# Kernel optimization log

Measured on AMD Instinct MI355X. Metric: run time of the kernel, lower is better.

Reference implementation:

```python
import jax, jax.numpy as jnp
import numpy as np

CUTOFFS = [16000, 28000, 36000]
HID = 1024
PROJ = [256, 64]  # hidden/4**1, hidden/4**2 per compute_proj_dims
CLUSTERS = 2


def setup_inputs() -> dict:
    key = jax.random.key(0)
    ks = jax.random.split(key, 12)
    B, S = 4, 1024
    scale = 0.02
    d = {
        "inp": jax.random.normal(ks[0], (B, S, HID), jnp.float32),
        "labels": jax.random.randint(ks[1], (B, S), 0, CUTOFFS[-1]),
        "head_W": jax.random.normal(ks[2], (HID, CUTOFFS[0] + CLUSTERS), jnp.float32) * scale,
        "head_b": jnp.zeros((CUTOFFS[0] + CLUSTERS,), jnp.float32),
    }
    for i in range(CLUSTERS):
        tdim = CUTOFFS[i + 1] - CUTOFFS[i]
        d[f"t{i}_pW"] = jax.random.normal(ks[3 + 4 * i], (HID, PROJ[i]), jnp.float32) * scale
        d[f"t{i}_pb"] = jnp.zeros((PROJ[i],), jnp.float32)
        d[f"t{i}_W"] = jax.random.normal(ks[4 + 4 * i], (PROJ[i], CUTOFFS[i + 1] - CUTOFFS[i]), jnp.float32) * scale
        d[f"t{i}_b"] = jnp.zeros((CUTOFFS[i + 1] - CUTOFFS[i],), jnp.float32)
    return d


def _sparse_ce(logits, labels):
    # stable sparse softmax cross entropy, single log_softmax pass
    logp = jax.nn.log_softmax(logits, axis=-1)
    return -jnp.take_along_axis(logp, labels[..., None], axis=-1)[..., 0]


def reference(inp, labels, head_W, head_b, t0_pW, t0_pb, t0_W, t0_b, t1_pW, t1_pb, t1_W, t1_b):
    tails = [(t0_pW, t0_pb, t0_W, t0_b), (t1_pW, t1_pb, t1_W, t1_b)]
    head_labels = labels
    loss = jnp.zeros(labels.shape, inp.dtype)
    for i, (pW, pb, W, b) in enumerate(tails):
        lo, hi = CUTOFFS[i], CUTOFFS[i + 1]
        mask = (labels >= lo) & (labels < hi)
        # tokens in cluster i are relabeled to cluster id in the head
        head_labels = jnp.where(mask, CUTOFFS[0] + i, head_labels)
        # two-layer tail projection: [B,S,H] -> [B,S,proj] -> [B,S,tail_dim]
        tail_logits = (inp @ pW + pb) @ W + b
        tail_labels = jnp.clip(labels - lo, 0, hi - lo - 1)
        loss = loss + jnp.where(mask, _sparse_ce(tail_logits, tail_labels), 0.0)
    head_logits = inp @ head_W + head_b  # [B,S,cutoffs[0]+clusters]
    loss = _sparse_ce(head_logits, head_labels) + loss
    loss = loss * (labels != 0).astype(loss.dtype)  # zero out pad positions
    return jnp.mean(loss)
```

## Files before the change

### kernel.cpp

```cpp
#include <hip/hip_runtime.h>
#include <hip/hip_bf16.h>
#include <hip/hip_fp8.h>
#include <cstdint>
#include <cstddef>

#define M_TOK 4096
#define HID   1024
#define NHEAD 16002
#define NHEAD_PAD 16128
#define P0    256
#define N0    12000
#define N0_PAD 12032
#define P1    64
#define N1    8000
#define N1_PAD 8192
#define PFUSE 384
#define PREAL 320

typedef unsigned char u8;
typedef float f32x4 __attribute__((ext_vector_type(4)));
typedef int   i32x4 __attribute__((ext_vector_type(4)));
typedef int   i32x8 __attribute__((ext_vector_type(8)));

__device__ __forceinline__ void load16(const void* g, void* l) {
    __builtin_amdgcn_global_load_lds(
        (__attribute__((address_space(1))) void*)g,
        (__attribute__((address_space(3))) void*)l,
        16, 0, 0);
}

__device__ __forceinline__ u8 to_e4m3(float f) {
    __hip_fp8_e4m3 h(f);
    return (u8)h.__x;
}

template <bool LSEP>
__device__ __forceinline__ void gemm_body(
        const u8* __restrict__ A, int lda, const u8* __restrict__ BT, int ldb,
        const float* __restrict__ bias, int K, int realN,
        const int* __restrict__ tgt, float* __restrict__ sumexp, float* __restrict__ lab,
        u8* __restrict__ out, int ldo, int m0, int n0,
        u8* As, u8* Bs) {
    const int tid  = threadIdx.x;
    const int lane = tid & 63;
    const int wave = tid >> 6;
    const int wm = wave >> 1, wn = wave & 1;
    const int q = lane >> 4, lrow = lane & 15;
    const int sw = lrow & 7;

    int aofs[4], bofs[4];
    #pragma unroll
    for (int p = 0; p < 4; p++) {
        int pg = wave * 256 + p * 64 + lane;
        int row = pg >> 3, gcol = (pg & 7) ^ (row & 7);
        aofs[p] = row * lda + gcol * 16;
        bofs[p] = row * ldb + gcol * 16;
    }

    f32x4 acc[4][4];
    #pragma unroll
    for (int mt = 0; mt < 4; mt++)
        #pragma unroll
        for (int nt = 0; nt < 4; nt++)
            acc[mt][nt] = (f32x4)(0.0f);

    const u8* Ab = A  + (size_t)m0 * lda;
    const u8* Bb = BT + (size_t)n0 * ldb;

    union Frag { struct { i32x4 lo, hi; } half; i32x8 v; };

    const int aLo = ((wm * 64 + lrow) * 8 + ((2 * q)     ^ sw)) * 16;
    const int aHi = ((wm * 64 + lrow) * 8 + ((2 * q + 1) ^ sw)) * 16;
    const int bLo = ((wn * 64 + lrow) * 8 + ((2 * q)     ^ sw)) * 16;
    const int bHi = ((wn * 64 + lrow) * 8 + ((2 * q + 1) ^ sw)) * 16;

    for (int k0 = 0; k0 < K; k0 += 128) {
        #pragma unroll
        for (int p = 0; p < 4; p++) {
            int base = (wave * 256 + p * 64) * 16;
            load16(Ab + k0 + aofs[p], As + base);
            load16(Bb + k0 + bofs[p], Bs + base);
        }
        __syncthreads();

        Frag fb[4];
        #pragma unroll
        for (int t = 0; t < 4; t++) {
            fb[t].half.lo = *reinterpret_cast<const i32x4*>(Bs + bLo + t * 2048);
            fb[t].half.hi = *reinterpret_cast<const i32x4*>(Bs + bHi + t * 2048);
        }
        Frag fA[2];
        fA[0].half.lo = *reinterpret_cast<const i32x4*>(As + aLo);
        fA[0].half.hi = *reinterpret_cast<const i32x4*>(As + aHi);
        #pragma unroll
        for (int mt = 0; mt < 4; mt++) {
            if (mt < 3) {
                fA[(mt + 1) & 1].half.lo = *reinterpret_cast<const i32x4*>(As + aLo + (mt + 1) * 2048);
                fA[(mt + 1) & 1].half.hi = *reinterpret_cast<const i32x4*>(As + aHi + (mt + 1) * 2048);
            }
            #pragma unroll
            for (int nt = 0; nt < 4; nt++)
                acc[mt][nt] = __builtin_amdgcn_mfma_scale_f32_16x16x128_f8f6f4(
                    fA[mt & 1].v, fb[nt].v, acc[mt][nt],
                    0, 0,
                    0, 0x7F7F7F7F,
                    0, 0x7A7A7A7A);
        }
        __syncthreads();
    }

    int colg[4]; float bias_v[4];
    #pragma unroll
    for (int nt = 0; nt < 4; nt++) {
        colg[nt] = n0 + wn * 64 + nt * 16 + lrow;
        bias_v[nt] = (colg[nt] < realN) ? bias[colg[nt]] : 0.0f;
    }

    #pragma unroll
    for (int mt = 0; mt < 4; mt++) {
        int rowb = m0 + wm * 64 + mt * 16 + q * 4;
        #pragma unroll
        for (int r = 0; r < 4; r++) {
            int tok = rowb + r;
            if constexpr (LSEP) {
                int tg = tgt[tok];
                float s = 0.0f;
                #pragma unroll
                for (int nt = 0; nt < 4; nt++) {
                    if (colg[nt] < realN) {
                        float logit = acc[mt][nt][r] + bias_v[nt];
                        s += __expf(logit);
                        if (colg[nt] == tg) atomicAdd(&lab[tok], logit);
                    }
                }
                s += __shfl_xor(s, 1);
                s += __shfl_xor(s, 2);
                s += __shfl_xor(s, 4);
                s += __shfl_xor(s, 8);
                if (lrow == 0) atomicAdd(&sumexp[tok], s);
            } else {
                #pragma unroll
                for (int nt = 0; nt < 4; nt++)
                    out[(size_t)tok * ldo + colg[nt]] = to_e4m3(acc[mt][nt][r] + bias_v[nt]);
            }
        }
    }
}

__launch_bounds__(256, 4)
__global__ void gemm_proj(const u8* __restrict__ A, const u8* __restrict__ BT,
                          const float* __restrict__ bias, u8* __restrict__ out) {
    __shared__ __align__(16) u8 As[16384];
    __shared__ __align__(16) u8 Bs[16384];
    gemm_body<false>(A, HID, BT, HID, bias, HID, PREAL,
                     nullptr, nullptr, nullptr, out, PFUSE,
                     blockIdx.x * 128, blockIdx.y * 128, As, Bs);
}

struct Seg {
    const u8* A; int lda;
    const u8* BT; int ldb;
    const float* bias; int K; int realN;
    const int* tgt; float* sumexp; float* lab;
    int nblk;
};

__launch_bounds__(256, 4)
__global__ void gemm_lse3(Seg s0, Seg s1, Seg s2) {
    __shared__ __align__(16) u8 As[16384];
    __shared__ __align__(16) u8 Bs[16384];
    int b = blockIdx.x;
    Seg s; int rel;
    if (b < s0.nblk)                { s = s0; rel = b; }
    else if (b < s0.nblk + s1.nblk) { s = s1; rel = b - s0.nblk; }
    else                            { s = s2; rel = b - s0.nblk - s1.nblk; }
    int pair = rel >> 6, inner = rel & 63;
    int m0 = (inner >> 1) * 128;
    int n0 = (pair * 2 + (inner & 1)) * 128;
    gemm_body<true>(s.A, s.lda, s.BT, s.ldb, s.bias, s.K, s.realN,
                    s.tgt, s.sumexp, s.lab, nullptr, 0, m0, n0, As, Bs);
}

__device__ __forceinline__ void do_transpose(const float* __restrict__ W, u8* __restrict__ WT,
                                             int K, int N, int Kpad, float scale,
                                             int bx, int by, float (*tile)[65]) {
    int n0 = bx * 64, k0 = by * 64;
    int tx = threadIdx.x & 63, ty = threadIdx.x >> 6;
    #pragma unroll
    for (int i = 0; i < 16; i++) {
        int k = k0 + ty + i * 4, n = n0 + tx;
        tile[ty + i * 4][tx] = (k < K && n < N) ? W[(size_t)k * N + n] * scale : 0.0f;
    }
    __syncthreads();
    int n = threadIdx.x >> 2, kb = (threadIdx.x & 3) * 16;
    union { u8 b[16]; uint4 u; } v;
    #pragma unroll
    for (int j = 0; j < 16; j++) v.b[j] = to_e4m3(tile[kb + j][n]);
    *reinterpret_cast<uint4*>(WT + (size_t)(n0 + n) * Kpad + k0 + kb) = v.u;
}

#define NBT_HEAD 4032
#define NBT_CAST 1024
#define NBT_T0W   752
#define NBT_T1W   256
#define NBT_T0P    64
#define NBT_T1P    32
#define NBT_INIT   16

__global__ void prep_kernel(const float* __restrict__ inp, const int* __restrict__ labels,
                            const float* __restrict__ head_W,
                            const float* __restrict__ t0_pW, const float* __restrict__ t0_pb,
                            const float* __restrict__ t0_W,
                            const float* __restrict__ t1_pW, const float* __restrict__ t1_pb,
                            const float* __restrict__ t1_W,
                            u8* __restrict__ inp_f8, u8* __restrict__ headW8,
                            u8* __restrict__ fpW8, u8* __restrict__ t0W8, u8* __restrict__ t1W8,
                            float* __restrict__ acc6, int* __restrict__ tgts,
                            float* __restrict__ pbias, float* __restrict__ out) {
    __shared__ float tile[64][65];
    int b = blockIdx.x;
    if (b < NBT_HEAD) {
        do_transpose(head_W, headW8, HID, NHEAD, HID, 32.0f, b % 252, b / 252, tile);
    } else if (b < NBT_HEAD + NBT_CAST) {
        int r = b - NBT_HEAD;
        int i = r * 256 + threadIdx.x;
        float4 v = reinterpret_cast<const float4*>(inp)[i];
        uchar4 o8;
        o8.x = to_e4m3(v.x); o8.y = to_e4m3(v.y); o8.z = to_e4m3(v.z); o8.w = to_e4m3(v.w);
        reinterpret_cast<uchar4*>(inp_f8)[i] = o8;
    } else if (b < NBT_HEAD + NBT_CAST + NBT_T0W) {
        int r = b - (NBT_HEAD + NBT_CAST);
        do_transpose(t0_W, t0W8, P0, N0, P0, 32.0f, r % 188, r / 188, tile);
    } else if (b < NBT_HEAD + NBT_CAST + NBT_T0W + NBT_T1W) {
        int r = b - (NBT_HEAD + NBT_CAST + NBT_T0W);
        do_transpose(t1_W, t1W8, P1, N1, 128, 32.0f, r % 128, r / 128, tile);
    } else if (b < NBT_HEAD + NBT_CAST + NBT_T0W + NBT_T1W + NBT_T0P) {
        int r = b - (NBT_HEAD + NBT_CAST + NBT_T0W + NBT_T1W);
        do_transpose(t0_pW, fpW8, HID, P0, HID, 32.0f, r % 4, r / 4, tile);
    } else if (b < NBT_HEAD + NBT_CAST + NBT_T0W + NBT_T1W + NBT_T0P + NBT_T1P) {
        int r = b - (NBT_HEAD + NBT_CAST + NBT_T0W + NBT_T1W + NBT_T0P);
        do_transpose(t1_pW, fpW8 + 256 * HID, HID, P1, HID, 32.0f, r % 2, r / 2, tile);
    } else {
        int r = b - (NBT_HEAD + NBT_CAST + NBT_T0W + NBT_T1W + NBT_T0P + NBT_T1P);
        int t = r * 256 + threadIdx.x;
        for (int j = t; j < 6 * M_TOK; j += M_TOK) acc6[j] = 0.0f;
        if (t == 0) out[0] = 0.0f;
        if (t < PFUSE) pbias[t] = (t < 256) ? t0_pb[t] : ((t < PREAL) ? t1_pb[t - 256] : 0.0f);
        int lbl = labels[t];
        tgts[t]             = (lbl < 16000) ? lbl : ((lbl < 28000) ? 16000 : 16001);
        int t0 = lbl - 16000; t0 = t0 < 0 ? 0 : (t0 > 11999 ? 11999 : t0);
        int t1 = lbl - 28000; t1 = t1 < 0 ? 0 : (t1 > 7999  ? 7999  : t1);
        tgts[M_TOK + t]     = t0;
        tgts[2 * M_TOK + t] = t1;
    }
}

__global__ void finalize_kernel(const int* __restrict__ labels, const float* __restrict__ acc6,
                                float* __restrict__ out) {
    int t = blockIdx.x * blockDim.x + threadIdx.x;
    const float* sumH = acc6;
    const float* labH = acc6 + M_TOK;
    const float* sum0 = acc6 + 2 * M_TOK;
    const float* lab0 = acc6 + 3 * M_TOK;
    const float* sum1 = acc6 + 4 * M_TOK;
    const float* lab1 = acc6 + 5 * M_TOK;
    int lbl = labels[t];
    float l = 0.0f;
    if (lbl != 0) {
        l = logf(sumH[t]) - labH[t];
        if (lbl >= 16000 && lbl < 28000) l += logf(sum0[t]) - lab0[t];
        else if (lbl >= 28000)           l += logf(sum1[t]) - lab1[t];
    }
    l *= (1.0f / (float)M_TOK);
    #pragma unroll
    for (int off = 1; off < 64; off <<= 1) l += __shfl_xor(l, off);
    __shared__ float red[4];
    if ((threadIdx.x & 63) == 0) red[threadIdx.x >> 6] = l;
    __syncthreads();
    if (threadIdx.x == 0) atomicAdd(out, red[0] + red[1] + red[2] + red[3]);
}

extern "C" void kernel_launch(void* const* d_in, const int* in_sizes, int n_in,
                              void* d_out, int out_size, void* d_ws, size_t ws_size,
                              hipStream_t stream) {
    const float* inp    = (const float*)d_in[0];
    const int*   labels = (const int*)  d_in[1];
    const float* head_W = (const float*)d_in[2];
    const float* head_b = (const float*)d_in[3];
    const float* t0_pW  = (const float*)d_in[4];
    const float* t0_pb  = (const float*)d_in[5];
    const float* t0_W   = (const float*)d_in[6];
    const float* t0_b   = (const float*)d_in[7];
    const float* t1_pW  = (const float*)d_in[8];
    const float* t1_pb  = (const float*)d_in[9];
    const float* t1_W   = (const float*)d_in[10];
    const float* t1_b   = (const float*)d_in[11];
    float* out = (float*)d_out;

    char* ws = (char*)d_ws;
    size_t off = 0;
    auto alloc = [&](size_t bytes) { char* p = ws + off; off += (bytes + 255) & ~(size_t)255; return p; };
    u8*    inp_f8  = (u8*)   alloc((size_t)M_TOK * HID);
    u8*    headW8  = (u8*)   alloc((size_t)NHEAD_PAD * HID);
    u8*    fpW8    = (u8*)   alloc((size_t)PFUSE * HID);
    u8*    t0W8    = (u8*)   alloc((size_t)N0_PAD * P0);
    u8*    t1W8    = (u8*)   alloc((size_t)N1_PAD * 128);
    u8*    proj8   = (u8*)   alloc((size_t)M_TOK * PFUSE);
    float* acc6    = (float*)alloc(6 * M_TOK * 4);
    int*   tgts    = (int*)  alloc(3 * M_TOK * 4);
    float* pbias   = (float*)alloc(PFUSE * 4);

    int nb = NBT_HEAD + NBT_CAST + NBT_T0W + NBT_T1W + NBT_T0P + NBT_T1P + NBT_INIT;
    prep_kernel<<<nb, 256, 0, stream>>>(inp, labels, head_W, t0_pW, t0_pb, t0_W,
                                        t1_pW, t1_pb, t1_W,
                                        inp_f8, headW8, fpW8, t0W8, t1W8,
                                        acc6, tgts, pbias, out);

    gemm_proj<<<dim3(M_TOK / 128, PFUSE / 128), 256, 0, stream>>>(inp_f8, fpW8, pbias, proj8);

    Seg s0{inp_f8,      HID,   headW8, HID, head_b, HID, NHEAD, tgts,             acc6,             acc6 + M_TOK,     32 * (NHEAD_PAD / 128)};
    Seg s1{proj8,       PFUSE, t0W8,   P0,  t0_b,   P0,  N0,    tgts + M_TOK,     acc6 + 2 * M_TOK, acc6 + 3 * M_TOK, 32 * (N0_PAD / 128)};
    Seg s2{proj8 + 256, PFUSE, t1W8,   128, t1_b,   128, N1,    tgts + 2 * M_TOK, acc6 + 4 * M_TOK, acc6 + 5 * M_TOK, 32 * (N1_PAD / 128)};
    gemm_lse3<<<s0.nblk + s1.nblk + s2.nblk, 256, 0, stream>>>(s0, s1, s2);

    finalize_kernel<<<M_TOK / 256, 256, 0, stream>>>(labels, acc6, out);
}
```

Baseline: 343.3 us.

## Load MFMA fragments directly from global memory and vectorize weight transpose loads

The FP8 GEMM body no longer stages A and B tiles through shared memory with global_load_lds and barriers. Each lane now reads its 32-byte MFMA fragments straight from global memory into registers, which removes LDS traffic and both __syncthreads per K step. The cost is that the two waves sharing an A or B tile each fetch it themselves, so reuse depends on L1/L2, and loads get no explicit prefetch overlap. Separately, the weight transpose/cast helper now reads float2 pairs per thread instead of scalar floats.

After: 509.7 us. +48.5%, slower.

```diff
diff --git a/kernel.cpp b/kernel.cpp
--- a/kernel.cpp
+++ b/kernel.cpp
@@ -22,13 +22,6 @@
 typedef int   i32x4 __attribute__((ext_vector_type(4)));
 typedef int   i32x8 __attribute__((ext_vector_type(8)));
 
-__device__ __forceinline__ void load16(const void* g, void* l) {
-    __builtin_amdgcn_global_load_lds(
-        (__attribute__((address_space(1))) void*)g,
-        (__attribute__((address_space(3))) void*)l,
-        16, 0, 0);
-}
-
 __device__ __forceinline__ u8 to_e4m3(float f) {
     __hip_fp8_e4m3 h(f);
     return (u8)h.__x;
@@ -39,23 +32,15 @@
         const u8* __restrict__ A, int lda, const u8* __restrict__ BT, int ldb,
         const float* __restrict__ bias, int K, int realN,
         const int* __restrict__ tgt, float* __restrict__ sumexp, float* __restrict__ lab,
-        u8* __restrict__ out, int ldo, int m0, int n0,
-        u8* As, u8* Bs) {
+        u8* __restrict__ out, int ldo, int m0, int n0) {
     const int tid  = threadIdx.x;
     const int lane = tid & 63;
     const int wave = tid >> 6;
     const int wm = wave >> 1, wn = wave & 1;
     const int q = lane >> 4, lrow = lane & 15;
-    const int sw = lrow & 7;
-
-    int aofs[4], bofs[4];
-    #pragma unroll
-    for (int p = 0; p < 4; p++) {
-        int pg = wave * 256 + p * 64 + lane;
-        int row = pg >> 3, gcol = (pg & 7) ^ (row & 7);
-        aofs[p] = row * lda + gcol * 16;
-        bofs[p] = row * ldb + gcol * 16;
-    }
+
+    const u8* Ap = A  + (size_t)(m0 + wm * 64 + lrow) * lda + q * 32;
+    const u8* Bp = BT + (size_t)(n0 + wn * 64 + lrow) * ldb + q * 32;
 
     f32x4 acc[4][4];
     #pragma unroll
@@ -64,49 +49,34 @@
         for (int nt = 0; nt < 4; nt++)
             acc[mt][nt] = (f32x4)(0.0f);
 
-    const u8* Ab = A  + (size_t)m0 * lda;
-    const u8* Bb = BT + (size_t)n0 * ldb;
-
     union Frag { struct { i32x4 lo, hi; } half; i32x8 v; };
 
-    const int aLo = ((wm * 64 + lrow) * 8 + ((2 * q)     ^ sw)) * 16;
-    const int aHi = ((wm * 64 + lrow) * 8 + ((2 * q + 1) ^ sw)) * 16;
-    const int bLo = ((wn * 64 + lrow) * 8 + ((2 * q)     ^ sw)) * 16;
-    const int bHi = ((wn * 64 + lrow) * 8 + ((2 * q + 1) ^ sw)) * 16;
-
     for (int k0 = 0; k0 < K; k0 += 128) {
-        #pragma unroll
-        for (int p = 0; p < 4; p++) {
-            int base = (wave * 256 + p * 64) * 16;
-            load16(Ab + k0 + aofs[p], As + base);
-            load16(Bb + k0 + bofs[p], Bs + base);
-        }
-        __syncthreads();
-
         Frag fb[4];
         #pragma unroll
-        for (int t = 0; t < 4; t++) {
-            fb[t].half.lo = *reinterpret_cast<const i32x4*>(Bs + bLo + t * 2048);
-            fb[t].half.hi = *reinterpret_cast<const i32x4*>(Bs + bHi + t * 2048);
+        for (int nt = 0; nt < 4; nt++) {
+            const u8* p = Bp + (size_t)nt * 16 * ldb + k0;
+            fb[nt].half.lo = *reinterpret_cast<const i32x4*>(p);
+            fb[nt].half.hi = *reinterpret_cast<const i32x4*>(p + 16);
         }
-        Frag fA[2];
-        fA[0].half.lo = *reinterpret_cast<const i32x4*>(As + aLo);
-        fA[0].half.hi = *reinterpret_cast<const i32x4*>(As + aHi);
+        Frag fa[2];
+        fa[0].half.lo = *reinterpret_cast<const i32x4*>(Ap + k0);
+        fa[0].half.hi = *reinterpret_cast<const i32x4*>(Ap + k0 + 16);
         #pragma unroll
         for (int mt = 0; mt < 4; mt++) {
             if (mt < 3) {
-                fA[(mt + 1) & 1].half.lo = *reinterpret_cast<const i32x4*>(As + aLo + (mt + 1) * 2048);
-                fA[(mt + 1) & 1].half.hi = *reinterpret_cast<const i32x4*>(As + aHi + (mt + 1) * 2048);
+                const u8* p = Ap + (size_t)(mt + 1) * 16 * lda + k0;
+                fa[(mt + 1) & 1].half.lo = *reinterpret_cast<const i32x4*>(p);
+                fa[(mt + 1) & 1].half.hi = *reinterpret_cast<const i32x4*>(p + 16);
             }
             #pragma unroll
             for (int nt = 0; nt < 4; nt++)
                 acc[mt][nt] = __builtin_amdgcn_mfma_scale_f32_16x16x128_f8f6f4(
-                    fA[mt & 1].v, fb[nt].v, acc[mt][nt],
+                    fa[mt & 1].v, fb[nt].v, acc[mt][nt],
                     0, 0,
                     0, 0x7F7F7F7F,
                     0, 0x7A7A7A7A);
         }
-        __syncthreads();
     }
 
     int colg[4]; float bias_v[4];
@@ -150,11 +120,9 @@
 __launch_bounds__(256, 4)
 __global__ void gemm_proj(const u8* __restrict__ A, const u8* __restrict__ BT,
                           const float* __restrict__ bias, u8* __restrict__ out) {
-    __shared__ __align__(16) u8 As[16384];
-    __shared__ __align__(16) u8 Bs[16384];
     gemm_body<false>(A, HID, BT, HID, bias, HID, PREAL,
                      nullptr, nullptr, nullptr, out, PFUSE,
-                     blockIdx.x * 128, blockIdx.y * 128, As, Bs);
+                     blockIdx.x * 128, blockIdx.y * 128);
 }
 
 struct Seg {
@@ -167,8 +135,6 @@
 
 __launch_bounds__(256, 4)
 __global__ void gemm_lse3(Seg s0, Seg s1, Seg s2) {
-    __shared__ __align__(16) u8 As[16384];
-    __shared__ __align__(16) u8 Bs[16384];
     int b = blockIdx.x;
     Seg s; int rel;
     if (b < s0.nblk)                { s = s0; rel = b; }
@@ -178,25 +144,35 @@
     int m0 = (inner >> 1) * 128;
     int n0 = (pair * 2 + (inner & 1)) * 128;
     gemm_body<true>(s.A, s.lda, s.BT, s.ldb, s.bias, s.K, s.realN,
-                    s.tgt, s.sumexp, s.lab, nullptr, 0, m0, n0, As, Bs);
+                    s.tgt, s.sumexp, s.lab, nullptr, 0, m0, n0);
 }
 
 __device__ __forceinline__ void do_transpose(const float* __restrict__ W, u8* __restrict__ WT,
                                              int K, int N, int Kpad, float scale,
                                              int bx, int by, float (*tile)[65]) {
     int n0 = bx * 64, k0 = by * 64;
-    int tx = threadIdx.x & 63, ty = threadIdx.x >> 6;
-    #pragma unroll
-    for (int i = 0; i < 16; i++) {
-        int k = k0 + ty + i * 4, n = n0 + tx;
-        tile[ty + i * 4][tx] = (k < K && n < N) ? W[(size_t)k * N + n] * scale : 0.0f;
+    int c2 = threadIdx.x & 31;
+    int rg = threadIdx.x >> 5;
+    int n = n0 + c2 * 2;
+    #pragma unroll
+    for (int j = 0; j < 8; j++) {
+        int k = k0 + rg + j * 8;
+        float2 v;
+        if (k < K && n + 1 < N) {
+            v = *reinterpret_cast<const float2*>(&W[(size_t)k * N + n]);
+        } else {
+            v.x = (k < K && n     < N) ? W[(size_t)k * N + n]     : 0.0f;
+            v.y = (k < K && n + 1 < N) ? W[(size_t)k * N + n + 1] : 0.0f;
+        }
+        tile[rg + j * 8][c2 * 2]     = v.x * scale;
+        tile[rg + j * 8][c2 * 2 + 1] = v.y * scale;
     }
     __syncthreads();
-    int n = threadIdx.x >> 2, kb = (threadIdx.x & 3) * 16;
+    int nn = threadIdx.x >> 2, kb = (threadIdx.x & 3) * 16;
     union { u8 b[16]; uint4 u; } v;
     #pragma unroll
-    for (int j = 0; j < 16; j++) v.b[j] = to_e4m3(tile[kb + j][n]);
-    *reinterpret_cast<uint4*>(WT + (size_t)(n0 + n) * Kpad + k0 + kb) = v.u;
+    for (int j = 0; j < 16; j++) v.b[j] = to_e4m3(tile[kb + j][nn]);
+    *reinterpret_cast<uint4*>(WT + (size_t)(n0 + nn) * Kpad + k0 + kb) = v.u;
 }
 
 #define NBT_HEAD 4032
```

## Use 512-thread GEMM blocks with 8 waves and LDS-reduced sumexp atomics

Applied to the files above, without the earlier changes.

The fp8 MFMA GEMM body now runs 8 waves per 128x128 tile. Each wave computes a 64x32 sub-tile instead of 64x64, which halves the accumulator count and is meant to raise occupancy and latency hiding. Per-row sumexp partials from the four column-waves are first summed in LDS and then written with a single atomic per row, cutting global atomic traffic. The weight transpose in prep now uses float2 loads. In exchange, each wave reads more A fragments from LDS per MFMA, and the launch bounds request an aggressive occupancy target.

Result: faster. 331.4 us (-3.5%).

```diff
diff --git a/kernel.cpp b/kernel.cpp
--- a/kernel.cpp
+++ b/kernel.cpp
@@ -44,64 +44,60 @@
     const int tid  = threadIdx.x;
     const int lane = tid & 63;
     const int wave = tid >> 6;
-    const int wm = wave >> 1, wn = wave & 1;
+    const int wm = wave >> 2, wn = wave & 3;
     const int q = lane >> 4, lrow = lane & 15;
     const int sw = lrow & 7;
 
-    int aofs[4], bofs[4];
-    #pragma unroll
-    for (int p = 0; p < 4; p++) {
-        int pg = wave * 256 + p * 64 + lane;
+    int aofs[2], bofs[2], lbase[2];
+    #pragma unroll
+    for (int p = 0; p < 2; p++) {
+        int pg = wave * 128 + p * 64 + lane;
         int row = pg >> 3, gcol = (pg & 7) ^ (row & 7);
-        aofs[p] = row * lda + gcol * 16;
-        bofs[p] = row * ldb + gcol * 16;
-    }
-
-    f32x4 acc[4][4];
+        aofs[p]  = row * lda + gcol * 16;
+        bofs[p]  = row * ldb + gcol * 16;
+        lbase[p] = (wave * 128 + p * 64) * 16;
+    }
+
+    f32x4 acc[4][2];
     #pragma unroll
     for (int mt = 0; mt < 4; mt++)
         #pragma unroll
-        for (int nt = 0; nt < 4; nt++)
+        for (int nt = 0; nt < 2; nt++)
             acc[mt][nt] = (f32x4)(0.0f);
 
     const u8* Ab = A  + (size_t)m0 * lda;
     const u8* Bb = BT + (size_t)n0 * ldb;
 
-    union Frag { struct { i32x4 lo, hi; } half; i32x8 v; };
-
     const int aLo = ((wm * 64 + lrow) * 8 + ((2 * q)     ^ sw)) * 16;
     const int aHi = ((wm * 64 + lrow) * 8 + ((2 * q + 1) ^ sw)) * 16;
-    const int bLo = ((wn * 64 + lrow) * 8 + ((2 * q)     ^ sw)) * 16;
-    const int bHi = ((wn * 64 + lrow) * 8 + ((2 * q + 1) ^ sw)) * 16;
+    const int bLo = ((wn * 32 + lrow) * 8 + ((2 * q)     ^ sw)) * 16;
+    const int bHi = ((wn * 32 + lrow) * 8 + ((2 * q + 1) ^ sw)) * 16;
+
+    union Frag { struct { i32x4 lo, hi; } half; i32x8 v; };
 
     for (int k0 = 0; k0 < K; k0 += 128) {
         #pragma unroll
-        for (int p = 0; p < 4; p++) {
-            int base = (wave * 256 + p * 64) * 16;
-            load16(Ab + k0 + aofs[p], As + base);
-            load16(Bb + k0 + bofs[p], Bs + base);
+        for (int p = 0; p < 2; p++) {
+            load16(Ab + k0 + aofs[p], As + lbase[p]);
+            load16(Bb + k0 + bofs[p], Bs + lbase[p]);
         }
         __syncthreads();
 
-        Frag fb[4];
-        #pragma unroll
-        for (int t = 0; t < 4; t++) {
+        Frag fb[2];
+        #pragma unroll
+        for (int t = 0; t < 2; t++) {
             fb[t].half.lo = *reinterpret_cast<const i32x4*>(Bs + bLo + t * 2048);
             fb[t].half.hi = *reinterpret_cast<const i32x4*>(Bs + bHi + t * 2048);
         }
-        Frag fA[2];
-        fA[0].half.lo = *reinterpret_cast<const i32x4*>(As + aLo);
-        fA[0].half.hi = *reinterpret_cast<const i32x4*>(As + aHi);
         #pragma unroll
         for (int mt = 0; mt < 4; mt++) {
-            if (mt < 3) {
-                fA[(mt + 1) & 1].half.lo = *reinterpret_cast<const i32x4*>(As + aLo + (mt + 1) * 2048);
-                fA[(mt + 1) & 1].half.hi = *reinterpret_cast<const i32x4*>(As + aHi + (mt + 1) * 2048);
-            }
+            Frag fa;
+            fa.half.lo = *reinterpret_cast<const i32x4*>(As + aLo + mt * 2048);
+            fa.half.hi = *reinterpret_cast<const i32x4*>(As + aHi + mt * 2048);
             #pragma unroll
-            for (int nt = 0; nt < 4; nt++)
+            for (int nt = 0; nt < 2; nt++)
                 acc[mt][nt] = __builtin_amdgcn_mfma_scale_f32_16x16x128_f8f6f4(
-                    fA[mt & 1].v, fb[nt].v, acc[mt][nt],
+                    fa.v, fb[nt].v, acc[mt][nt],
                     0, 0,
                     0, 0x7F7F7F7F,
                     0, 0x7A7A7A7A);
@@ -109,12 +105,14 @@
         __syncthreads();
     }
 
-    int colg[4]; float bias_v[4];
-    #pragma unroll
-    for (int nt = 0; nt < 4; nt++) {
-        colg[nt] = n0 + wn * 64 + nt * 16 + lrow;
+    int colg[2]; float bias_v[2];
+    #pragma unroll
+    for (int nt = 0; nt < 2; nt++) {
+        colg[nt] = n0 + wn * 32 + nt * 16 + lrow;
         bias_v[nt] = (colg[nt] < realN) ? bias[colg[nt]] : 0.0f;
     }
+
+    float* sred = reinterpret_cast<float*>(As);
 
     #pragma unroll
     for (int mt = 0; mt < 4; mt++) {
@@ -126,7 +124,7 @@
                 int tg = tgt[tok];
                 float s = 0.0f;
                 #pragma unroll
-                for (int nt = 0; nt < 4; nt++) {
+                for (int nt = 0; nt < 2; nt++) {
                     if (colg[nt] < realN) {
                         float logit = acc[mt][nt][r] + bias_v[nt];
                         s += __expf(logit);
@@ -137,17 +135,25 @@
                 s += __shfl_xor(s, 2);
                 s += __shfl_xor(s, 4);
                 s += __shfl_xor(s, 8);
-                if (lrow == 0) atomicAdd(&sumexp[tok], s);
+                if (lrow == 0) sred[wn * 128 + (wm * 64 + mt * 16 + q * 4 + r)] = s;
             } else {
                 #pragma unroll
-                for (int nt = 0; nt < 4; nt++)
+                for (int nt = 0; nt < 2; nt++)
                     out[(size_t)tok * ldo + colg[nt]] = to_e4m3(acc[mt][nt][r] + bias_v[nt]);
             }
         }
     }
-}
-
-__launch_bounds__(256, 4)
+
+    if constexpr (LSEP) {
+        __syncthreads();
+        if (tid < 128) {
+            float v = sred[tid] + sred[128 + tid] + sred[256 + tid] + sred[384 + tid];
+            atomicAdd(&sumexp[m0 + tid], v);
+        }
+    }
+}
+
+__launch_bounds__(512, 6)
 __global__ void gemm_proj(const u8* __restrict__ A, const u8* __restrict__ BT,
                           const float* __restrict__ bias, u8* __restrict__ out) {
     __shared__ __align__(16) u8 As[16384];
@@ -165,7 +171,7 @@
     int nblk;
 };
 
-__launch_bounds__(256, 4)
+__launch_bounds__(512, 6)
 __global__ void gemm_lse3(Seg s0, Seg s1, Seg s2) {
     __shared__ __align__(16) u8 As[16384];
     __shared__ __align__(16) u8 Bs[16384];
@@ -185,18 +191,28 @@
                                              int K, int N, int Kpad, float scale,
                                              int bx, int by, float (*tile)[65]) {
     int n0 = bx * 64, k0 = by * 64;
-    int tx = threadIdx.x & 63, ty = threadIdx.x >> 6;
-    #pragma unroll
-    for (int i = 0; i < 16; i++) {
-        int k = k0 + ty + i * 4, n = n0 + tx;
-        tile[ty + i * 4][tx] = (k < K && n < N) ? W[(size_t)k * N + n] * scale : 0.0f;
+    int c2 = threadIdx.x & 31;
+    int rg = threadIdx.x >> 5;
+    int n = n0 + c2 * 2;
+    #pragma unroll
+    for (int j = 0; j < 8; j++) {
+        int k = k0 + rg + j * 8;
+        float2 v;
+        if (k < K && n + 1 < N) {
+            v = *reinterpret_cast<const float2*>(&W[(size_t)k * N + n]);
+        } else {
+            v.x = (k < K && n     < N) ? W[(size_t)k * N + n]     : 0.0f;
+            v.y = (k < K && n + 1 < N) ? W[(size_t)k * N + n + 1] : 0.0f;
+        }
+        tile[rg + j * 8][c2 * 2]     = v.x * scale;
+        tile[rg + j * 8][c2 * 2 + 1] = v.y * scale;
     }
     __syncthreads();
-    int n = threadIdx.x >> 2, kb = (threadIdx.x & 3) * 16;
+    int nn = threadIdx.x >> 2, kb = (threadIdx.x & 3) * 16;
     union { u8 b[16]; uint4 u; } v;
     #pragma unroll
-    for (int j = 0; j < 16; j++) v.b[j] = to_e4m3(tile[kb + j][n]);
-    *reinterpret_cast<uint4*>(WT + (size_t)(n0 + n) * Kpad + k0 + kb) = v.u;
+    for (int j = 0; j < 16; j++) v.b[j] = to_e4m3(tile[kb + j][nn]);
+    *reinterpret_cast<uint4*>(WT + (size_t)(n0 + nn) * Kpad + k0 + kb) = v.u;
 }
 
 #define NBT_HEAD 4032
@@ -316,12 +332,12 @@
                                         inp_f8, headW8, fpW8, t0W8, t1W8,
                                         acc6, tgts, pbias, out);
 
-    gemm_proj<<<dim3(M_TOK / 128, PFUSE / 128), 256, 0, stream>>>(inp_f8, fpW8, pbias, proj8);
+    gemm_proj<<<dim3(M_TOK / 128, PFUSE / 128), 512, 0, stream>>>(inp_f8, fpW8, pbias, proj8);
 
     Seg s0{inp_f8,      HID,   headW8, HID, head_b, HID, NHEAD, tgts,             acc6,             acc6 + M_TOK,     32 * (NHEAD_PAD / 128)};
     Seg s1{proj8,       PFUSE, t0W8,   P0,  t0_b,   P0,  N0,    tgts + M_TOK,     acc6 + 2 * M_TOK, acc6 + 3 * M_TOK, 32 * (N0_PAD / 128)};
     Seg s2{proj8 + 256, PFUSE, t1W8,   128, t1_b,   128, N1,    tgts + 2 * M_TOK, acc6 + 4 * M_TOK, acc6 + 5 * M_TOK, 32 * (N1_PAD / 128)};
-    gemm_lse3<<<s0.nblk + s1.nblk + s2.nblk, 256, 0, stream>>>(s0, s1, s2);
+    gemm_lse3<<<s0.nblk + s1.nblk + s2.nblk, 512, 0, stream>>>(s0, s1, s2);
 
     finalize_kernel<<<M_TOK / 256, 256, 0, stream>>>(labels, acc6, out);
 }
```
